# Kernel tuning notes

Hardware: AMD Instinct MI355X
Metric: run time of the kernel (lower is better)

Reference implementation:

```python
import jax, jax.numpy as jnp
import numpy as np
from jax import lax

C = 128        # args.feat_dim
HF = WF = 320  # feature map spatial size
IMG = 1280     # segmentation map resolution
N = 256        # number of anchors
CROP = 32      # fixed crop size (h and w)
NUM_CLASSES = 151
NUM_BASE = 64


def setup_inputs() -> dict:
    key = jax.random.key(0)
    ks = jax.random.split(key, 9)
    feature_map = jax.random.normal(ks[0], (C, HF, WF), dtype=jnp.float32)
    seg = jax.random.randint(ks[1], (IMG, IMG), 0, NUM_CLASSES, dtype=jnp.int32)
    x0 = jax.random.randint(ks[2], (N,), 0, WF - CROP, dtype=jnp.int32)
    y0 = jax.random.randint(ks[3], (N,), 0, HF - CROP, dtype=jnp.int32)
    # anchors layout matches torch code: [x0, x1, y0, y1] in feature-map pixels
    anchors = jnp.stack([x0, x0 + CROP, y0, y0 + CROP], axis=1)
    labels = jax.random.randint(ks[4], (N,), 0, NUM_BASE, dtype=jnp.int32)
    base_classes = jax.random.randint(ks[5], (NUM_BASE,), 0, NUM_CLASSES, dtype=jnp.int32)
    W1 = jax.random.normal(ks[6], (256, C, 3, 3), dtype=jnp.float32) * 0.02
    b1 = jnp.zeros((256,), dtype=jnp.float32)
    W2 = jax.random.normal(ks[7], (1, 256, 3, 3), dtype=jnp.float32) * 0.02
    b2 = jnp.zeros((1,), dtype=jnp.float32)
    return {"feature_map": feature_map, "seg": seg, "anchors": anchors,
            "labels": labels, "base_classes": base_classes,
            "W1": W1, "b1": b1, "W2": W2, "b2": b2}


def reference(feature_map, seg, anchors, labels, base_classes, W1, b1, W2, b2):
    # F.interpolate(mode='nearest') from IMGxIMG down to HFxWF: idx = floor(i * in/out)
    hi = (jnp.arange(HF) * seg.shape[0]) // HF
    wi = (jnp.arange(WF) * seg.shape[1]) // WF
    mask = seg[hi][:, wi].astype(jnp.float32)  # [HF, WF]

    starts = anchors[:, jnp.array([2, 0])]  # (h0, w0) per anchor

    def crop_feat(s):
        return lax.dynamic_slice(feature_map, (jnp.int32(0), s[0], s[1]), (C, CROP, CROP))

    def crop_mask(s):
        return lax.dynamic_slice(mask, (s[0], s[1]), (CROP, CROP))

    crops = jax.vmap(crop_feat)(starts)       # [N, C, CROP, CROP]
    mask_crops = jax.vmap(crop_mask)(starts)  # [N, CROP, CROP]

    dn = ('NCHW', 'OIHW', 'NCHW')
    h = lax.conv_general_dilated(crops, W1, (1, 1), 'SAME', dimension_numbers=dn)
    h = jax.nn.relu(h + b1[None, :, None, None])
    logits = lax.conv_general_dilated(h, W2, (1, 1), 'SAME', dimension_numbers=dn)
    logits = logits + b2[None, :, None, None]  # [N, 1, CROP, CROP]

    tgt_cls = base_classes[labels].astype(jnp.float32)  # [N]
    tgt = (mask_crops == tgt_cls[:, None, None]).astype(jnp.float32)[:, None]  # [N,1,CROP,CROP]

    # stable BCE-with-logits: max(x,0) - x*t + log1p(exp(-|x|))
    bce = jnp.maximum(logits, 0.0) - logits * tgt + jnp.log1p(jnp.exp(-jnp.abs(logits)))
    per_anchor = bce.mean(axis=(1, 2, 3))  # mean per anchor, as in F.binary_cross_entropy_with_logits
    return per_anchor.sum() / (N + 1e-10)
```

## Files before the change

### kernel.cpp

```cpp
#include <hip/hip_runtime.h>

typedef __attribute__((ext_vector_type(8))) short short8;
typedef __attribute__((ext_vector_type(8))) int int8v;
typedef __attribute__((ext_vector_type(16))) float floatx16;
typedef __attribute__((ext_vector_type(4))) unsigned int uint4v;
typedef unsigned short ushort_t;
typedef unsigned int uint_t;
typedef unsigned char uchar_t;

#define NA   256
#define CIN  128
#define HFD  320
#define FMPX (HFD*HFD)
#define IMGD 1280

#define W1R_BYTE_OFF (1u<<20)
#define W2R_BYTE_OFF ((1u<<20) + 9*256*128)
#define FMT_BYTE_OFF (2u<<20)

#define SAPL 9792
#define SBPL 9216
#define SA_BYTES (4*SAPL)
#define SB_BYTES (4*SBPL)
#define PSTR_H 8208

union V32 { int8v v; uint4v q[2]; };

__device__ __forceinline__ ushort_t f2bf(float v) {
    uint_t u = __float_as_uint(v);
    return (ushort_t)((u + 0x8000u) >> 16);
}
__device__ __forceinline__ uchar_t f2fp8(float v) {
    int r = __builtin_amdgcn_cvt_pk_fp8_f32(v, 0.0f, 0, false);
    return (uchar_t)(r & 0xff);
}

__global__ __launch_bounds__(256) void prep_misc(
    const float* __restrict__ W1, const float* __restrict__ W2,
    float* __restrict__ logits, float* __restrict__ out,
    uchar_t* __restrict__ w1r, ushort_t* __restrict__ w2r)
{
    const int b = blockIdx.x, t = threadIdx.x;
    if (b < 1024) {
        logits[b * 256 + t] = 0.0f;
    } else if (b < 1024 + 128) {
        int e = (b - 1024) * 256 + t;
        int oc = e >> 7, cin = e & 127;
        #pragma unroll
        for (int tap = 0; tap < 9; ++tap)
            w1r[(tap * 256 + oc) * 128 + cin] = f2fp8(W1[(oc * 128 + cin) * 9 + tap] * 64.0f);
    } else {
        #pragma unroll
        for (int i = 0; i < 32; ++i) {
            int e = i * 256 + t;
            int nrow = e >> 8, oc = e & 255;
            w2r[nrow * 256 + oc] = f2bf(nrow < 9 ? W2[oc * 9 + nrow] : 0.0f);
        }
        if (t == 0) out[0] = 0.0f;
    }
}

__global__ __launch_bounds__(256) void prep_transpose(
    const float* __restrict__ fm, uchar_t* __restrict__ fmT)
{
    __shared__ uchar_t s[32 * 144];
    const int t = threadIdx.x;
    const int y = blockIdx.y, x0b = blockIdx.x * 32;
    #pragma unroll
    for (int i = 0; i < 16; ++i) {
        int e = t + 256 * i;
        int c = e >> 5, xo = e & 31;
        s[xo * 144 + c] = f2fp8(fm[(size_t)c * FMPX + y * HFD + x0b + xo]);
    }
    __syncthreads();
    {
        int xo = t >> 3, cg = t & 7;
        uint4v v = *(const uint4v*)&s[xo * 144 + cg * 16];
        *(uint4v*)&fmT[((size_t)(y * HFD + x0b + xo)) * 128 + cg * 16] = v;
    }
}

__global__ __launch_bounds__(256, 2) void conv_mfma_kernel(
    const int* __restrict__ anchors, const uchar_t* __restrict__ fmT,
    const uchar_t* __restrict__ w1r, const ushort_t* __restrict__ w2r,
    const float* __restrict__ b1, float* __restrict__ logits)
{
    const int id   = blockIdx.x;
    const int xcd  = id & 7, sid = id >> 3;
    const int n    = xcd * 32 + (sid >> 3);
    const int rem  = sid & 7;
    const int half = rem >> 2;
    const int g    = rem & 3;

    const int t    = threadIdx.x;
    const int w    = t >> 6;
    const int lane = t & 63;
    const int l31  = lane & 31;
    const int kh   = lane >> 5;

    const int x0 = anchors[n * 4 + 0];
    const int y0 = anchors[n * 4 + 2];
    const int r0 = half * 16;
    const int pro = 1 - half;

    __shared__ __align__(16) char smem[SA_BYTES + SB_BYTES];
    char* s_a = smem;
    char* s_b = smem + SA_BYTES;
    __shared__ float s_log[18 * 32];

    for (int i = t; i < SA_BYTES / 4; i += 256) ((uint_t*)s_a)[i] = 0u;

    floatx16 acc[4][2];
    #pragma unroll
    for (int mt = 0; mt < 4; ++mt)
        #pragma unroll
        for (int nt = 0; nt < 2; ++nt)
            #pragma unroll
            for (int r = 0; r < 16; ++r) acc[mt][nt][r] = 0.0f;

    for (int c = 0; c < 2; ++c) {
        const int cb = c * 64;
        __syncthreads();
        #pragma unroll
        for (int j = 0; j < 9; ++j) {
            int u = t + 256 * j;
            if (j < 8 || u < 2176) {
                int cell = u >> 2, sub = u & 3;
                int ri = cell >> 5, col = cell & 31;
                int pr = ri + pro, cr = r0 + pr - 1;
                uint4v v = *(const uint4v*)&fmT[((size_t)((y0 + cr) * HFD + x0 + col)) * 128 + cb + sub * 16];
                *(uint4v*)(s_a + sub * SAPL + (pr * 34 + col + 1) * 16) = v;
            }
        }
        #pragma unroll
        for (int j = 0; j < 9; ++j) {
            int u = t + 256 * j;
            int cell = u >> 2, sub = u & 3;
            int tap = cell >> 6, oc = cell & 63;
            uint4v v = *(const uint4v*)&w1r[(size_t)((tap * 256 + g * 64 + oc) * 128) + cb + sub * 16];
            *(uint4v*)(s_b + sub * SBPL + cell * 16) = v;
        }
        __syncthreads();
        #pragma unroll
        for (int kx = 0; kx < 3; ++kx) {
            V32 a8[6];
            #pragma unroll
            for (int r = 0; r < 6; ++r) {
                int cell = (4 * w + r) * 34 + l31 + kx;
                a8[r].q[0] = *(const uint4v*)(s_a + (2 * kh)     * SAPL + cell * 16);
                a8[r].q[1] = *(const uint4v*)(s_a + (2 * kh + 1) * SAPL + cell * 16);
            }
            #pragma unroll
            for (int ky = 0; ky < 3; ++ky) {
                int tap = ky * 3 + kx;
                V32 b8[2];
                #pragma unroll
                for (int nt = 0; nt < 2; ++nt) {
                    int cell = tap * 64 + nt * 32 + l31;
                    b8[nt].q[0] = *(const uint4v*)(s_b + (2 * kh)     * SBPL + cell * 16);
                    b8[nt].q[1] = *(const uint4v*)(s_b + (2 * kh + 1) * SBPL + cell * 16);
                }
                #pragma unroll
                for (int mt = 0; mt < 4; ++mt) {
                    acc[mt][0] = __builtin_amdgcn_mfma_scale_f32_32x32x64_f8f6f4(
                        a8[mt + ky].v, b8[0].v, acc[mt][0], 0, 0, 0, 127, 0, 127);
                    acc[mt][1] = __builtin_amdgcn_mfma_scale_f32_32x32x64_f8f6f4(
                        a8[mt + ky].v, b8[1].v, acc[mt][1], 0, 0, 0, 127, 0, 127);
                }
            }
        }
    }

    __syncthreads();
    #pragma unroll
    for (int pass = 0; pass < 2; ++pass) {
        float bias = b1[g * 64 + pass * 32 + l31];
        int plane = pass * 4 + (l31 >> 3);
        #pragma unroll
        for (int mt = 0; mt < 4; ++mt) {
            int lr = 4 * w + mt;
            #pragma unroll
            for (int reg = 0; reg < 16; ++reg) {
                int col = (reg & 3) + 8 * (reg >> 2) + 4 * kh;
                float hv = fmaxf(fmaf(acc[mt][pass][reg], 0.015625f, bias), 0.0f);
                *(ushort_t*)(smem + plane * PSTR_H + ((lr * 32 + col) * 8 + (l31 & 7)) * 2) = f2bf(hv);
            }
        }
    }
    __syncthreads();

    floatx16 vacc[4];
    #pragma unroll
    for (int mt = 0; mt < 4; ++mt)
        #pragma unroll
        for (int r = 0; r < 16; ++r) vacc[mt][r] = 0.0f;
    #pragma unroll
    for (int ks = 0; ks < 4; ++ks) {
        short8 bw = *(const short8*)&w2r[l31 * 256 + g * 64 + ks * 16 + kh * 8];
        #pragma unroll
        for (int mt = 0; mt < 4; ++mt) {
            short8 ah = *(const short8*)(smem + (ks * 2 + kh) * PSTR_H + ((4 * w + mt) * 32 + l31) * 16);
            vacc[mt] = __builtin_amdgcn_mfma_f32_32x32x16_bf16(ah, bw, vacc[mt], 0, 0, 0);
        }
    }

    __syncthreads();
    for (int i = t; i < 18 * 32; i += 256) s_log[i] = 0.0f;
    __syncthreads();
    if (l31 < 9) {
        int ky = l31 / 3, kx = l31 - ky * 3;
        #pragma unroll
        for (int mt = 0; mt < 4; ++mt) {
            int outr = 4 * w + mt + 2 - ky;
            #pragma unroll
            for (int reg = 0; reg < 16; ++reg) {
                int col  = (reg & 3) + 8 * (reg >> 2) + 4 * kh;
                int outc = col + 1 - kx;
                if (outc >= 0 && outc < 32)
                    atomicAdd(&s_log[outr * 32 + outc], vacc[mt][reg]);
            }
        }
    }
    __syncthreads();
    for (int i = t; i < 18 * 32; i += 256) {
        int outr = i >> 5, outc = i & 31;
        int R = r0 + outr - 1;
        if ((unsigned)R < 32u)
            atomicAdd(&logits[n * 1024 + R * 32 + outc], s_log[i]);
    }
}

__global__ __launch_bounds__(256) void bce_reduce_kernel(
    const float* __restrict__ logits, const int* __restrict__ seg,
    const int* __restrict__ anchors, const int* __restrict__ labels,
    const int* __restrict__ base_classes, const float* __restrict__ b2,
    float* __restrict__ out)
{
    const int n = blockIdx.x;
    const int t = threadIdx.x;
    const int y0 = anchors[n * 4 + 2];
    const int x0 = anchors[n * 4 + 0];
    const int tgt_cls = base_classes[labels[n]];
    const float bias2 = b2[0];

    float lsum = 0.0f;
    #pragma unroll
    for (int r = 0; r < 4; ++r) {
        int p = t + r * 256;
        int i = p >> 5, j = p & 31;
        float l = logits[n * 1024 + p] + bias2;
        int sv = seg[(size_t)(4 * (y0 + i)) * IMGD + 4 * (x0 + j)];
        float tgt = (sv == tgt_cls) ? 1.0f : 0.0f;
        lsum += fmaxf(l, 0.0f) - l * tgt + log1pf(expf(-fabsf(l)));
    }
    #pragma unroll
    for (int off = 32; off > 0; off >>= 1) lsum += __shfl_down(lsum, off, 64);
    __shared__ float s[4];
    if ((t & 63) == 0) s[t >> 6] = lsum;
    __syncthreads();
    if (t == 0) {
        float tot = s[0] + s[1] + s[2] + s[3];
        const float scale = 1.0f / (1024.0f * (256.0f + 1e-10f));
        atomicAdd(out, tot * scale);
    }
}

extern "C" void kernel_launch(void* const* d_in, const int* in_sizes, int n_in,
                              void* d_out, int out_size, void* d_ws, size_t ws_size,
                              hipStream_t stream) {
    const float* fm           = (const float*)d_in[0];
    const int*   seg          = (const int*)d_in[1];
    const int*   anchors      = (const int*)d_in[2];
    const int*   labels       = (const int*)d_in[3];
    const int*   base_classes = (const int*)d_in[4];
    const float* W1           = (const float*)d_in[5];
    const float* b1           = (const float*)d_in[6];
    const float* W2           = (const float*)d_in[7];
    const float* b2           = (const float*)d_in[8];
    float* out = (float*)d_out;

    float*    logits = (float*)d_ws;
    uchar_t*  w1r    = (uchar_t*)((char*)d_ws + W1R_BYTE_OFF);
    ushort_t* w2r    = (ushort_t*)((char*)d_ws + W2R_BYTE_OFF);
    uchar_t*  fmT    = (uchar_t*)((char*)d_ws + FMT_BYTE_OFF);

    prep_misc<<<1024 + 128 + 1, 256, 0, stream>>>(W1, W2, logits, out, w1r, w2r);
    prep_transpose<<<dim3(10, 320), 256, 0, stream>>>(fm, fmT);
    conv_mfma_kernel<<<2048, 256, 0, stream>>>(anchors, fmT, w1r, w2r, b1, logits);
    bce_reduce_kernel<<<NA, 256, 0, stream>>>(logits, seg, anchors, labels, base_classes, b2, out);
}
```

Measured before the change: 230.6 us.

## Split conv tiles into quarter-row blocks, read weights directly in MFMA-ready layout

```diff
diff --git a/kernel.cpp b/kernel.cpp
--- a/kernel.cpp
+++ b/kernel.cpp
@@ -18,11 +18,8 @@
 #define W2R_BYTE_OFF ((1u<<20) + 9*256*128)
 #define FMT_BYTE_OFF (2u<<20)
 
-#define SAPL 9792
-#define SBPL 9216
-#define SA_BYTES (4*SAPL)
-#define SB_BYTES (4*SBPL)
-#define PSTR_H 8208
+#define SAPL_Q 5440
+#define PSTR_Q 4112
 
 union V32 { int8v v; uint4v q[2]; };
 
@@ -38,7 +35,7 @@
 __global__ __launch_bounds__(256) void prep_misc(
     const float* __restrict__ W1, const float* __restrict__ W2,
     float* __restrict__ logits, float* __restrict__ out,
-    uchar_t* __restrict__ w1r, ushort_t* __restrict__ w2r)
+    uchar_t* __restrict__ w1b, ushort_t* __restrict__ w2r)
 {
     const int b = blockIdx.x, t = threadIdx.x;
     if (b < 1024) {
@@ -46,9 +43,13 @@
     } else if (b < 1024 + 128) {
         int e = (b - 1024) * 256 + t;
         int oc = e >> 7, cin = e & 127;
-        #pragma unroll
-        for (int tap = 0; tap < 9; ++tap)
-            w1r[(tap * 256 + oc) * 128 + cin] = f2fp8(W1[(oc * 128 + cin) * 9 + tap] * 64.0f);
+        int g = oc >> 6, nt = (oc >> 5) & 1, lv = oc & 31;
+        int c = cin >> 6, kh = (cin >> 5) & 1, j = cin & 31;
+        #pragma unroll
+        for (int tap = 0; tap < 9; ++tap) {
+            int idx = (((((tap * 4 + g) * 2 + nt) * 2 + c) * 64) + kh * 32 + lv) * 32 + j;
+            w1b[idx] = f2fp8(W1[(oc * 128 + cin) * 9 + tap] * 64.0f);
+        }
     } else {
         #pragma unroll
         for (int i = 0; i < 32; ++i) {
@@ -80,16 +81,16 @@
     }
 }
 
-__global__ __launch_bounds__(256, 2) void conv_mfma_kernel(
+__global__ __launch_bounds__(256, 4) void conv_mfma_kernel(
     const int* __restrict__ anchors, const uchar_t* __restrict__ fmT,
-    const uchar_t* __restrict__ w1r, const ushort_t* __restrict__ w2r,
+    const uchar_t* __restrict__ w1b, const ushort_t* __restrict__ w2r,
     const float* __restrict__ b1, float* __restrict__ logits)
 {
     const int id   = blockIdx.x;
     const int xcd  = id & 7, sid = id >> 3;
-    const int n    = xcd * 32 + (sid >> 3);
-    const int rem  = sid & 7;
-    const int half = rem >> 2;
+    const int n    = xcd * 32 + (sid >> 4);
+    const int rem  = sid & 15;
+    const int q    = rem >> 2;
     const int g    = rem & 3;
 
     const int t    = threadIdx.x;
@@ -100,72 +101,65 @@
 
     const int x0 = anchors[n * 4 + 0];
     const int y0 = anchors[n * 4 + 2];
-    const int r0 = half * 16;
-    const int pro = 1 - half;
-
-    __shared__ __align__(16) char smem[SA_BYTES + SB_BYTES];
+    const int r0 = q * 8;
+
+    __shared__ __align__(16) char smem[8 * PSTR_Q];
     char* s_a = smem;
-    char* s_b = smem + SA_BYTES;
-    __shared__ float s_log[18 * 32];
-
-    for (int i = t; i < SA_BYTES / 4; i += 256) ((uint_t*)s_a)[i] = 0u;
-
-    floatx16 acc[4][2];
-    #pragma unroll
-    for (int mt = 0; mt < 4; ++mt)
+
+    if (t < 80) {
+        int sub = t & 3, k = t >> 2;
+        int pr = k >> 1, col = (k & 1) * 33;
+        uint4v z = {0u, 0u, 0u, 0u};
+        *(uint4v*)(s_a + sub * SAPL_Q + (pr * 34 + col) * 16) = z;
+    }
+
+    floatx16 acc[2][2];
+    #pragma unroll
+    for (int mt = 0; mt < 2; ++mt)
         #pragma unroll
         for (int nt = 0; nt < 2; ++nt)
             #pragma unroll
             for (int r = 0; r < 16; ++r) acc[mt][nt][r] = 0.0f;
 
     for (int c = 0; c < 2; ++c) {
-        const int cb = c * 64;
         __syncthreads();
         #pragma unroll
-        for (int j = 0; j < 9; ++j) {
+        for (int j = 0; j < 5; ++j) {
             int u = t + 256 * j;
-            if (j < 8 || u < 2176) {
-                int cell = u >> 2, sub = u & 3;
-                int ri = cell >> 5, col = cell & 31;
-                int pr = ri + pro, cr = r0 + pr - 1;
-                uint4v v = *(const uint4v*)&fmT[((size_t)((y0 + cr) * HFD + x0 + col)) * 128 + cb + sub * 16];
-                *(uint4v*)(s_a + sub * SAPL + (pr * 34 + col + 1) * 16) = v;
-            }
-        }
-        #pragma unroll
-        for (int j = 0; j < 9; ++j) {
-            int u = t + 256 * j;
-            int cell = u >> 2, sub = u & 3;
-            int tap = cell >> 6, oc = cell & 63;
-            uint4v v = *(const uint4v*)&w1r[(size_t)((tap * 256 + g * 64 + oc) * 128) + cb + sub * 16];
-            *(uint4v*)(s_b + sub * SBPL + cell * 16) = v;
+            int pr = u >> 7, rr = u & 127;
+            int cell = rr >> 2, sub = rr & 3;
+            int cr = r0 + pr - 1;
+            uint4v v = {0u, 0u, 0u, 0u};
+            if ((unsigned)cr < 32u)
+                v = *(const uint4v*)&fmT[((size_t)((y0 + cr) * HFD + x0 + cell)) * 128 + c * 64 + sub * 16];
+            *(uint4v*)(s_a + sub * SAPL_Q + (pr * 34 + cell + 1) * 16) = v;
         }
         __syncthreads();
         #pragma unroll
         for (int kx = 0; kx < 3; ++kx) {
-            V32 a8[6];
-            #pragma unroll
-            for (int r = 0; r < 6; ++r) {
-                int cell = (4 * w + r) * 34 + l31 + kx;
-                a8[r].q[0] = *(const uint4v*)(s_a + (2 * kh)     * SAPL + cell * 16);
-                a8[r].q[1] = *(const uint4v*)(s_a + (2 * kh + 1) * SAPL + cell * 16);
-            }
             #pragma unroll
             for (int ky = 0; ky < 3; ++ky) {
-                int tap = ky * 3 + kx;
+                const int tap = ky * 3 + kx;
                 V32 b8[2];
                 #pragma unroll
                 for (int nt = 0; nt < 2; ++nt) {
-                    int cell = tap * 64 + nt * 32 + l31;
-                    b8[nt].q[0] = *(const uint4v*)(s_b + (2 * kh)     * SBPL + cell * 16);
-                    b8[nt].q[1] = *(const uint4v*)(s_b + (2 * kh + 1) * SBPL + cell * 16);
+                    const uchar_t* bp = w1b + ((((tap * 4 + g) * 2 + nt) * 2 + c) << 11) + lane * 32;
+                    b8[nt].q[0] = *(const uint4v*)(bp);
+                    b8[nt].q[1] = *(const uint4v*)(bp + 16);
+                }
+                V32 a2[2];
+                #pragma unroll
+                for (int f = 0; f < 2; ++f) {
+                    int cell = (2 * w + ky + f) * 34 + l31 + kx;
+                    a2[f].q[0] = *(const uint4v*)(s_a + (2 * kh)     * SAPL_Q + cell * 16);
+                    a2[f].q[1] = *(const uint4v*)(s_a + (2 * kh + 1) * SAPL_Q + cell * 16);
                 }
                 #pragma unroll
-                for (int mt = 0; mt < 4; ++mt) {
+                for (int mt = 0; mt < 2; ++mt) {
                     acc[mt][0] = __builtin_amdgcn_mfma_scale_f32_32x32x64_f8f6f4(
-                        a8[mt + ky].v, b8[0].v, acc[mt][0], 0, 0, 0, 127, 0, 127);
+                        a2[mt].v, b8[0].v, acc[mt][0], 0, 0, 0, 127, 0, 127);
                     acc[mt][1] = __builtin_amdgcn_mfma_scale_f32_32x32x64_f8f6f4(
-                        a8[mt + ky].v, b8[1].v, acc[mt][1], 0, 0, 0, 127, 0, 127);
+                        a2[mt].v, b8[1].v, acc[mt][1], 0, 0, 0, 127, 0, 127);
                 }
             }
         }
@@ -173,45 +167,46 @@
 
     __syncthreads();
     #pragma unroll
-    for (int pass = 0; pass < 2; ++pass) {
-        float bias = b1[g * 64 + pass * 32 + l31];
-        int plane = pass * 4 + (l31 >> 3);
-        #pragma unroll
-        for (int mt = 0; mt < 4; ++mt) {
-            int lr = 4 * w + mt;
+    for (int nt = 0; nt < 2; ++nt) {
+        float bias = b1[g * 64 + nt * 32 + l31];
+        int plane = nt * 4 + (l31 >> 3);
+        #pragma unroll
+        for (int mt = 0; mt < 2; ++mt) {
+            int lr = 2 * w + mt;
             #pragma unroll
             for (int reg = 0; reg < 16; ++reg) {
                 int col = (reg & 3) + 8 * (reg >> 2) + 4 * kh;
-                float hv = fmaxf(fmaf(acc[mt][pass][reg], 0.015625f, bias), 0.0f);
-                *(ushort_t*)(smem + plane * PSTR_H + ((lr * 32 + col) * 8 + (l31 & 7)) * 2) = f2bf(hv);
+                float hv = fmaxf(fmaf(acc[mt][nt][reg], 0.015625f, bias), 0.0f);
+                *(ushort_t*)(smem + plane * PSTR_Q + ((lr * 32 + col) * 8 + (l31 & 7)) * 2) = f2bf(hv);
             }
         }
     }
     __syncthreads();
 
-    floatx16 vacc[4];
-    #pragma unroll
-    for (int mt = 0; mt < 4; ++mt)
+    floatx16 vacc[2];
+    #pragma unroll
+    for (int mt = 0; mt < 2; ++mt)
         #pragma unroll
         for (int r = 0; r < 16; ++r) vacc[mt][r] = 0.0f;
     #pragma unroll
     for (int ks = 0; ks < 4; ++ks) {
         short8 bw = *(const short8*)&w2r[l31 * 256 + g * 64 + ks * 16 + kh * 8];
         #pragma unroll
-        for (int mt = 0; mt < 4; ++mt) {
-            short8 ah = *(const short8*)(smem + (ks * 2 + kh) * PSTR_H + ((4 * w + mt) * 32 + l31) * 16);
+        for (int mt = 0; mt < 2; ++mt) {
+            short8 ah = *(const short8*)(smem + (ks * 2 + kh) * PSTR_Q + ((2 * w + mt) * 32 + l31) * 16);
             vacc[mt] = __builtin_amdgcn_mfma_f32_32x32x16_bf16(ah, bw, vacc[mt], 0, 0, 0);
         }
     }
 
     __syncthreads();
-    for (int i = t; i < 18 * 32; i += 256) s_log[i] = 0.0f;
+    float* s_log = (float*)smem;
+    for (int i = t; i < 320; i += 256) s_log[i] = 0.0f;
     __syncthreads();
     if (l31 < 9) {
         int ky = l31 / 3, kx = l31 - ky * 3;
         #pragma unroll
-        for (int mt = 0; mt < 4; ++mt) {
-            int outr = 4 * w + mt + 2 - ky;
+        for (int mt = 0; mt < 2; ++mt) {
+            int outr = 2 * w + mt + 2 - ky;
             #pragma unroll
             for (int reg = 0; reg < 16; ++reg) {
                 int col  = (reg & 3) + 8 * (reg >> 2) + 4 * kh;
@@ -222,7 +217,7 @@
         }
     }
     __syncthreads();
-    for (int i = t; i < 18 * 32; i += 256) {
+    for (int i = t; i < 320; i += 256) {
         int outr = i >> 5, outc = i & 31;
         int R = r0 + outr - 1;
         if ((unsigned)R < 32u)
@@ -280,12 +275,12 @@
     float* out = (float*)d_out;
 
     float*    logits = (float*)d_ws;
-    uchar_t*  w1r    = (uchar_t*)((char*)d_ws + W1R_BYTE_OFF);
+    uchar_t*  w1b    = (uchar_t*)((char*)d_ws + W1R_BYTE_OFF);
     ushort_t* w2r    = (ushort_t*)((char*)d_ws + W2R_BYTE_OFF);
     uchar_t*  fmT    = (uchar_t*)((char*)d_ws + FMT_BYTE_OFF);
 
-    prep_misc<<<1024 + 128 + 1, 256, 0, stream>>>(W1, W2, logits, out, w1r, w2r);
+    prep_misc<<<1024 + 128 + 1, 256, 0, stream>>>(W1, W2, logits, out, w1b, w2r);
     prep_transpose<<<dim3(10, 320), 256, 0, stream>>>(fm, fmT);
-    conv_mfma_kernel<<<2048, 256, 0, stream>>>(anchors, fmT, w1r, w2r, b1, logits);
+    conv_mfma_kernel<<<4096, 256, 0, stream>>>(anchors, fmT, w1b, w2r, b1, logits);
     bce_reduce_kernel<<<NA, 256, 0, stream>>>(logits, seg, anchors, labels, base_classes, b2, out);
 }
```

Measured after the change: 321.6 us. +39.5%, slower.
